# Kernel optimization log

Hardware: AMD Instinct MI355X
Metric: run time of the kernel (lower is better)

Reference implementation:

```python
import jax, jax.numpy as jnp
import numpy as np

INPUT_SIZE = 300
HIDDEN = 128
NUM_CLASSES = 2
B, T = 256, 512


def setup_inputs() -> dict:
    key = jax.random.key(0)
    ks = jax.random.split(key, 7)
    s_ih = 1.0 / np.sqrt(HIDDEN)
    x = jax.random.normal(ks[0], (B, T, INPUT_SIZE), dtype=jnp.float32)
    W_ih = jax.random.uniform(ks[1], (HIDDEN, INPUT_SIZE), minval=-s_ih, maxval=s_ih, dtype=jnp.float32)
    W_hh = jax.random.uniform(ks[2], (HIDDEN, HIDDEN), minval=-s_ih, maxval=s_ih, dtype=jnp.float32)
    b_ih = jax.random.uniform(ks[3], (HIDDEN,), minval=-s_ih, maxval=s_ih, dtype=jnp.float32)
    b_hh = jax.random.uniform(ks[4], (HIDDEN,), minval=-s_ih, maxval=s_ih, dtype=jnp.float32)
    fc_w = jax.random.uniform(ks[5], (NUM_CLASSES, HIDDEN), minval=-s_ih, maxval=s_ih, dtype=jnp.float32)
    fc_b = jax.random.uniform(ks[6], (NUM_CLASSES,), minval=-s_ih, maxval=s_ih, dtype=jnp.float32)
    return {"x": x, "W_ih": W_ih, "W_hh": W_hh, "b_ih": b_ih, "b_hh": b_hh, "fc_w": fc_w, "fc_b": fc_b}


def reference(x, W_ih, W_hh, b_ih, b_hh, fc_w, fc_b):
    # Precompute input projections for all timesteps: [B,T,H]
    xp = jnp.einsum('bti,hi->bth', x, W_ih) + b_ih + b_hh
    h0 = jnp.zeros((x.shape[0], HIDDEN), dtype=x.dtype)

    def step(h, xp_t):  # xp_t: [B,H]
        h_new = jnp.tanh(xp_t + h @ W_hh.T)
        return h_new, None

    h_last, _ = jax.lax.scan(step, h0, jnp.swapaxes(xp, 0, 1))  # scan over T
    # Final FC on last hidden state (out[:, -1, :] of the RNN outputs)
    return h_last @ fc_w.T + fc_b
```

## Files before the change

kernel.cpp:

```cpp
#include <hip/hip_runtime.h>
#include <cstdint>
#include <cstddef>

#define KIN 300
#define KPAD 320
#define HIDDEN 128
#define BSZ 256
#define TSZ 512

#define ASTR 332

typedef __attribute__((ext_vector_type(8))) short short8;
typedef __attribute__((ext_vector_type(4))) short s16x4;
typedef __attribute__((ext_vector_type(4))) float f32x4;

__device__ __forceinline__ short f2bf(float f) {
  uint32_t u = __builtin_bit_cast(uint32_t, f);
  u = (u + 0x7FFFu + ((u >> 16) & 1u)) >> 16;
  return (short)u;
}
__device__ __forceinline__ float bf2f(short s) {
  uint32_t u = ((uint32_t)(uint16_t)s) << 16;
  return __builtin_bit_cast(float, u);
}
__device__ __forceinline__ float bflo(uint32_t u) {
  return __builtin_bit_cast(float, u << 16);
}
__device__ __forceinline__ float bfhi(uint32_t u) {
  return __builtin_bit_cast(float, u & 0xFFFF0000u);
}
__device__ __forceinline__ uint32_t pack2bf(float a, float b) {
  uint32_t r;
  asm("v_cvt_pk_bf16_f32 %0, %1, %2" : "=v"(r) : "v"(a), "v"(b));
  return r;
}
__device__ __forceinline__ float tanhf_fast(float v) {
  const float e = __builtin_amdgcn_exp2f(v * 2.88539008177793f);
  return fmaf(-2.0f, __builtin_amdgcn_rcpf(e + 1.0f), 1.0f);
}
__device__ __forceinline__ void barrier_lds() {
  asm volatile("s_waitcnt lgkmcnt(0)\n\ts_barrier" ::: "memory");
}
__device__ __forceinline__ void barrier_all() {
  asm volatile("s_waitcnt vmcnt(0) lgkmcnt(0)\n\ts_barrier" ::: "memory");
}
__device__ __forceinline__ void dma16(const short* g, short* l) {
  __builtin_amdgcn_global_load_lds(
      (const __attribute__((address_space(1))) void*)g,
      (__attribute__((address_space(3))) void*)l, 16, 0, 0);
}
__device__ __forceinline__ short8 ld_bh(const short* lo) {
  const s16x4 a = *(const s16x4*)lo;
  const s16x4 b = *(const s16x4*)(lo + 64);
  return __builtin_shufflevector(a, b, 0, 1, 2, 3, 4, 5, 6, 7);
}

__global__ __launch_bounds__(256) void wcvt_bf16(const float* __restrict__ W,
                                                 short* __restrict__ W16) {
  const int i = blockIdx.x * 256 + threadIdx.x;
  if (i >= HIDDEN * KPAD) return;
  const int n = i / KPAD, k = i % KPAD;
  W16[i] = (k < KIN) ? f2bf(W[n * KIN + k]) : (short)0;
}

__global__ __launch_bounds__(256) void xp_gemm_mfma(
    const float* __restrict__ x, const short* __restrict__ W16,
    const float* __restrict__ b_ih, const float* __restrict__ b_hh,
    short* __restrict__ xp16) {
  __shared__ __align__(16) short As[64 * ASTR];
  const int tid = threadIdx.x;
  const int lane = tid & 63, w = tid >> 6;
  const int q = lane >> 4, c = lane & 15;
  const int bg = blockIdx.x & 15, tc = blockIdx.x >> 4;
  const int b0 = bg * 16, t0 = tc * 4;

#pragma unroll
  for (int i = 0; i < 19; ++i) {
    const int f = tid + 256 * i;
    if (f < 4800) {
      const int rr = f / 75;
      const int k4 = f - rr * 75;
      const int b_in = rr >> 2, t_loc = rr & 3;
      const float4 v = *(const float4*)(
          x + ((size_t)(b0 + b_in) * TSZ + t0 + t_loc) * KIN + k4 * 4);
      uint2 pv;
      pv.x = pack2bf(v.x, v.y);
      pv.y = pack2bf(v.z, v.w);
      *(uint2*)&As[rr * ASTR + k4 * 4] = pv;
    }
  }
  if (tid < 64) {
    const uint2 z = {0u, 0u};
#pragma unroll
    for (int j = 0; j < 5; ++j) *(uint2*)&As[tid * ASTR + 300 + j * 4] = z;
  }
  __syncthreads();

  f32x4 acc[2][4];
#pragma unroll
  for (int ht = 0; ht < 2; ++ht)
#pragma unroll
    for (int rt = 0; rt < 4; ++rt) acc[ht][rt] = (f32x4){0.f, 0.f, 0.f, 0.f};

  const short* wp0 = W16 + (size_t)((2 * w + 0) * 16 + c) * KPAD + q * 8;
  const short* wp1 = W16 + (size_t)((2 * w + 1) * 16 + c) * KPAD + q * 8;
  const short* bqp = &As[c * ASTR + q * 8];
  short8 af[2][2];
  short8 bq[2][4];
  af[0][0] = *(const short8*)(wp0);
  af[0][1] = *(const short8*)(wp1);
#pragma unroll
  for (int rt = 0; rt < 4; ++rt)
    bq[0][rt] = *(const short8*)(bqp + rt * 16 * ASTR);
#pragma unroll
  for (int kc = 0; kc < 10; ++kc) {
    const int cur = kc & 1;
    if (kc < 9) {
      af[cur ^ 1][0] = *(const short8*)(wp0 + (kc + 1) * 32);
      af[cur ^ 1][1] = *(const short8*)(wp1 + (kc + 1) * 32);
#pragma unroll
      for (int rt = 0; rt < 4; ++rt)
        bq[cur ^ 1][rt] = *(const short8*)(bqp + rt * 16 * ASTR + (kc + 1) * 32);
    }
#pragma unroll
    for (int ht = 0; ht < 2; ++ht)
#pragma unroll
      for (int rt = 0; rt < 4; ++rt)
        acc[ht][rt] = __builtin_amdgcn_mfma_f32_16x16x32_bf16(
            af[cur][ht], bq[cur][rt], acc[ht][rt], 0, 0, 0);
  }
  __syncthreads();

  float4 bsum[2];
#pragma unroll
  for (int ht = 0; ht < 2; ++ht) {
    const int h0 = (2 * w + ht) * 16 + q * 4;
    const float4 bi = *(const float4*)(b_ih + h0);
    const float4 bh = *(const float4*)(b_hh + h0);
    bsum[ht] = make_float4(bi.x + bh.x, bi.y + bh.y, bi.z + bh.z, bi.w + bh.w);
  }
#pragma unroll
  for (int ht = 0; ht < 2; ++ht) {
    const int g = (2 * w + ht) * 4 + q;
#pragma unroll
    for (int rt = 0; rt < 4; ++rt) {
      const int b_in = rt * 4 + (c >> 2);
      const int t_loc = c & 3;
      uint2 pv;
      pv.x = pack2bf(acc[ht][rt][0] + bsum[ht].x, acc[ht][rt][1] + bsum[ht].y);
      pv.y = pack2bf(acc[ht][rt][2] + bsum[ht].z, acc[ht][rt][3] + bsum[ht].w);
      *(uint2*)&As[t_loc * 2312 + g * 72 + b_in * 4] = pv;
    }
  }
  __syncthreads();
#pragma unroll
  for (int i = 0; i < 4; ++i) {
    const int4 vv =
        *(const int4*)&As[i * 2312 + (tid >> 3) * 72 + (tid & 7) * 8];
    *(int4*)(xp16 + ((size_t)(t0 + i) * 16 + bg) * 2048 + tid * 8) = vv;
  }
}

__global__ __launch_bounds__(512, 2) void rnn_scan_dma(
    const short* __restrict__ xp16, const float* __restrict__ Whh,
    const float* __restrict__ fc_w, const float* __restrict__ fc_b,
    float* __restrict__ out) {
  __shared__ __align__(16) short xs[2][8][2048];
  __shared__ __align__(16) short ht[2][16][132];
  const int tid = threadIdx.x;
  const int lane = tid & 63, w = tid >> 6;
  const int q = lane >> 4, c = lane & 15;
  const int bg = blockIdx.x;

  short8 aw[4];
#pragma unroll
  for (int kc = 0; kc < 4; ++kc) {
    const float* src = Whh + (size_t)(w * 16 + c) * HIDDEN + kc * 32 + q * 8;
    const float4 v0 = *(const float4*)(src);
    const float4 v1 = *(const float4*)(src + 4);
    short8 t;
    t[0] = f2bf(v0.x); t[1] = f2bf(v0.y); t[2] = f2bf(v0.z); t[3] = f2bf(v0.w);
    t[4] = f2bf(v1.x); t[5] = f2bf(v1.y); t[6] = f2bf(v1.z); t[7] = f2bf(v1.w);
    aw[kc] = t;
  }

  {
    uint32_t* z = (uint32_t*)&ht[0][0][0];
    for (int i = tid; i < 2112; i += 512) z[i] = 0;
  }

#define ISSUE_CHUNK(CH, BUF)                                                  \
  {                                                                           \
    const short* srcb =                                                       \
        xp16 + ((size_t)((CH)*8 + w) * 16 + bg) * 2048 + lane * 8;            \
    _Pragma("unroll") for (int j = 0; j < 4; ++j)                             \
        dma16(srcb + j * 512, &xs[BUF][w][j * 512]);                          \
  }

  ISSUE_CHUNK(0, 0)
  barrier_all();

  const int gx = (w * 4 + q) * 64 + c * 4;
  const int cb = (q & 1) * 64 + (2 * w + (q >> 1)) * 4;
  const short* bhp0 = &ht[0][c][4 * q];
  const short* bhp1 = &ht[1][c][4 * q];

  for (int cc = 0; cc < 64; ++cc) {
    const int buf = cc & 1;
    if (cc + 1 < 64) ISSUE_CHUNK(cc + 1, buf ^ 1)
    uint2 us[8];
#pragma unroll
    for (int s = 0; s < 8; ++s) us[s] = *(const uint2*)&xs[buf][s][gx];
#pragma unroll
    for (int s = 0; s < 8; ++s) {
      const int rb = s & 1;
      const short* bp = rb ? bhp1 : bhp0;
      const short8 bh0 = ld_bh(bp + 0);
      const short8 bh1 = ld_bh(bp + 16);
      const short8 bh2 = ld_bh(bp + 32);
      const short8 bh3 = ld_bh(bp + 48);
      f32x4 a0 = {bflo(us[s].x), bfhi(us[s].x), bflo(us[s].y), bfhi(us[s].y)};
      f32x4 a2 = {0.f, 0.f, 0.f, 0.f};
      a0 = __builtin_amdgcn_mfma_f32_16x16x32_bf16(aw[0], bh0, a0, 0, 0, 0);
      a2 = __builtin_amdgcn_mfma_f32_16x16x32_bf16(aw[2], bh2, a2, 0, 0, 0);
      a0 = __builtin_amdgcn_mfma_f32_16x16x32_bf16(aw[1], bh1, a0, 0, 0, 0);
      a2 = __builtin_amdgcn_mfma_f32_16x16x32_bf16(aw[3], bh3, a2, 0, 0, 0);
      const f32x4 s0 = a0 + a2;
      uint2 w0;
      w0.x = pack2bf(tanhf_fast(s0[0]), tanhf_fast(s0[1]));
      w0.y = pack2bf(tanhf_fast(s0[2]), tanhf_fast(s0[3]));
      *(uint2*)&ht[rb ^ 1][c][cb] = w0;
      barrier_lds();
    }
    barrier_all();
  }
#undef ISSUE_CHUNK

  if (tid < 32) {
    const int bi = tid >> 1, cls = tid & 1;
    float s = fc_b[cls];
    const float* fw = fc_w + cls * HIDDEN;
#pragma unroll 4
    for (int g8 = 0; g8 < 16; ++g8) {
#pragma unroll
      for (int j = 0; j < 4; ++j) {
        s = fmaf(bf2f(ht[0][bi][g8 * 4 + j]), fw[g8 * 8 + j], s);
        s = fmaf(bf2f(ht[0][bi][64 + g8 * 4 + j]), fw[g8 * 8 + 4 + j], s);
      }
    }
    out[(bg * 16 + bi) * 2 + cls] = s;
  }
}

extern "C" void kernel_launch(void* const* d_in, const int* in_sizes, int n_in,
                              void* d_out, int out_size, void* d_ws, size_t ws_size,
                              hipStream_t stream) {
  const float* x    = (const float*)d_in[0];
  const float* W_ih = (const float*)d_in[1];
  const float* W_hh = (const float*)d_in[2];
  const float* b_ih = (const float*)d_in[3];
  const float* b_hh = (const float*)d_in[4];
  const float* fc_w = (const float*)d_in[5];
  const float* fc_b = (const float*)d_in[6];
  short* xp16 = (short*)d_ws;
  short* W16  = (short*)((char*)d_ws + (33u << 20));
  float* out  = (float*)d_out;

  wcvt_bf16<<<(HIDDEN * KPAD + 255) / 256, 256, 0, stream>>>(W_ih, W16);
  xp_gemm_mfma<<<16 * (TSZ / 4), 256, 0, stream>>>(x, W16, b_ih, b_hh, xp16);
  rnn_scan_dma<<<16, 512, 0, stream>>>(xp16, W_hh, fc_w, fc_b, out);
}
```

Baseline: 445.9 us.

## Fuse input projection GEMM and RNN scan into one kernel with flag handoff

After: 533.6 us. 19.7% more time.

```diff
diff --git a/kernel.cpp b/kernel.cpp
--- a/kernel.cpp
+++ b/kernel.cpp
@@ -41,9 +41,6 @@
 __device__ __forceinline__ void barrier_lds() {
   asm volatile("s_waitcnt lgkmcnt(0)\n\ts_barrier" ::: "memory");
 }
-__device__ __forceinline__ void barrier_all() {
-  asm volatile("s_waitcnt vmcnt(0) lgkmcnt(0)\n\ts_barrier" ::: "memory");
-}
 __device__ __forceinline__ void dma16(const short* g, short* l) {
   __builtin_amdgcn_global_load_lds(
       (const __attribute__((address_space(1))) void*)g,
@@ -54,123 +51,136 @@
   const s16x4 b = *(const s16x4*)(lo + 64);
   return __builtin_shufflevector(a, b, 0, 1, 2, 3, 4, 5, 6, 7);
 }
-
-__global__ __launch_bounds__(256) void wcvt_bf16(const float* __restrict__ W,
-                                                 short* __restrict__ W16) {
-  const int i = blockIdx.x * 256 + threadIdx.x;
-  if (i >= HIDDEN * KPAD) return;
-  const int n = i / KPAD, k = i % KPAD;
-  W16[i] = (k < KIN) ? f2bf(W[n * KIN + k]) : (short)0;
-}
-
-__global__ __launch_bounds__(256) void xp_gemm_mfma(
-    const float* __restrict__ x, const short* __restrict__ W16,
-    const float* __restrict__ b_ih, const float* __restrict__ b_hh,
-    short* __restrict__ xp16) {
-  __shared__ __align__(16) short As[64 * ASTR];
+__device__ __forceinline__ short8 ldWfrag(const float* __restrict__ W, int row,
+                                          int k0) {
+  short8 t;
+  const float* p = W + (size_t)row * KIN + k0;
+  if (k0 + 8 <= KIN) {
+    const float4 v0 = *(const float4*)(p);
+    const float4 v1 = *(const float4*)(p + 4);
+    t[0] = f2bf(v0.x); t[1] = f2bf(v0.y); t[2] = f2bf(v0.z); t[3] = f2bf(v0.w);
+    t[4] = f2bf(v1.x); t[5] = f2bf(v1.y); t[6] = f2bf(v1.z); t[7] = f2bf(v1.w);
+  } else {
+#pragma unroll
+    for (int j = 0; j < 8; ++j) {
+      const int k = k0 + j;
+      t[j] = (k < KIN) ? f2bf(p[j]) : (short)0;
+    }
+  }
+  return t;
+}
+
+union SMemU {
+  short As[64 * ASTR];
+  struct {
+    short xs[3][8][2048];
+    short ht[2][16][132];
+  } c;
+};
+
+__global__ __launch_bounds__(512, 1) void rnn_fused(
+    const float* __restrict__ x, const float* __restrict__ Wih,
+    const float* __restrict__ Whh, const float* __restrict__ b_ih,
+    const float* __restrict__ b_hh, const float* __restrict__ fc_w,
+    const float* __restrict__ fc_b, short* __restrict__ xp16,
+    int* __restrict__ flags, float* __restrict__ out) {
+  __shared__ __align__(16) union SMemU sm;
   const int tid = threadIdx.x;
   const int lane = tid & 63, w = tid >> 6;
   const int q = lane >> 4, c = lane & 15;
-  const int bg = blockIdx.x & 15, tc = blockIdx.x >> 4;
-  const int b0 = bg * 16, t0 = tc * 4;
-
-#pragma unroll
-  for (int i = 0; i < 19; ++i) {
-    const int f = tid + 256 * i;
-    if (f < 4800) {
-      const int rr = f / 75;
-      const int k4 = f - rr * 75;
-      const int b_in = rr >> 2, t_loc = rr & 3;
-      const float4 v = *(const float4*)(
-          x + ((size_t)(b0 + b_in) * TSZ + t0 + t_loc) * KIN + k4 * 4);
-      uint2 pv;
-      pv.x = pack2bf(v.x, v.y);
-      pv.y = pack2bf(v.z, v.w);
-      *(uint2*)&As[rr * ASTR + k4 * 4] = pv;
-    }
-  }
-  if (tid < 64) {
-    const uint2 z = {0u, 0u};
-#pragma unroll
-    for (int j = 0; j < 5; ++j) *(uint2*)&As[tid * ASTR + 300 + j * 4] = z;
-  }
-  __syncthreads();
-
-  f32x4 acc[2][4];
-#pragma unroll
-  for (int ht = 0; ht < 2; ++ht)
-#pragma unroll
-    for (int rt = 0; rt < 4; ++rt) acc[ht][rt] = (f32x4){0.f, 0.f, 0.f, 0.f};
-
-  const short* wp0 = W16 + (size_t)((2 * w + 0) * 16 + c) * KPAD + q * 8;
-  const short* wp1 = W16 + (size_t)((2 * w + 1) * 16 + c) * KPAD + q * 8;
-  const short* bqp = &As[c * ASTR + q * 8];
-  short8 af[2][2];
-  short8 bq[2][4];
-  af[0][0] = *(const short8*)(wp0);
-  af[0][1] = *(const short8*)(wp1);
-#pragma unroll
-  for (int rt = 0; rt < 4; ++rt)
-    bq[0][rt] = *(const short8*)(bqp + rt * 16 * ASTR);
-#pragma unroll
-  for (int kc = 0; kc < 10; ++kc) {
-    const int cur = kc & 1;
-    if (kc < 9) {
-      af[cur ^ 1][0] = *(const short8*)(wp0 + (kc + 1) * 32);
-      af[cur ^ 1][1] = *(const short8*)(wp1 + (kc + 1) * 32);
+
+  if (blockIdx.x >= 16) {
+    const int pid = blockIdx.x - 16;
+    const int bg = pid & 15, tc = pid >> 4;
+    const int b0 = bg * 16, t0 = tc * 4;
+    short* As = sm.As;
+
+#pragma unroll
+    for (int i = 0; i < 10; ++i) {
+      const int f = tid + 512 * i;
+      if (f < 4800) {
+        const int rr = f / 75;
+        const int k4 = f - rr * 75;
+        const int b_in = rr >> 2, t_loc = rr & 3;
+        const float4 v = *(const float4*)(
+            x + ((size_t)(b0 + b_in) * TSZ + t0 + t_loc) * KIN + k4 * 4);
+        uint2 pv;
+        pv.x = pack2bf(v.x, v.y);
+        pv.y = pack2bf(v.z, v.w);
+        *(uint2*)&As[rr * ASTR + k4 * 4] = pv;
+      }
+    }
+    if (tid < 64) {
+      const uint2 z = {0u, 0u};
+#pragma unroll
+      for (int j = 0; j < 5; ++j) *(uint2*)&As[tid * ASTR + 300 + j * 4] = z;
+    }
+    __syncthreads();
+
+    f32x4 acc[4];
+#pragma unroll
+    for (int rt = 0; rt < 4; ++rt) acc[rt] = (f32x4){0.f, 0.f, 0.f, 0.f};
+    const int row = w * 16 + c;
+    const short* bqp = &As[c * ASTR + q * 8];
+    short8 af[2];
+    short8 bq[2][4];
+    af[0] = ldWfrag(Wih, row, q * 8);
+#pragma unroll
+    for (int rt = 0; rt < 4; ++rt)
+      bq[0][rt] = *(const short8*)(bqp + rt * 16 * ASTR);
+#pragma unroll
+    for (int kc = 0; kc < 10; ++kc) {
+      const int cur = kc & 1;
+      if (kc < 9) {
+        af[cur ^ 1] = ldWfrag(Wih, row, (kc + 1) * 32 + q * 8);
+#pragma unroll
+        for (int rt = 0; rt < 4; ++rt)
+          bq[cur ^ 1][rt] =
+              *(const short8*)(bqp + rt * 16 * ASTR + (kc + 1) * 32);
+      }
 #pragma unroll
       for (int rt = 0; rt < 4; ++rt)
-        bq[cur ^ 1][rt] = *(const short8*)(bqp + rt * 16 * ASTR + (kc + 1) * 32);
-    }
-#pragma unroll
-    for (int ht = 0; ht < 2; ++ht)
-#pragma unroll
-      for (int rt = 0; rt < 4; ++rt)
-        acc[ht][rt] = __builtin_amdgcn_mfma_f32_16x16x32_bf16(
-            af[cur][ht], bq[cur][rt], acc[ht][rt], 0, 0, 0);
-  }
-  __syncthreads();
-
-  float4 bsum[2];
-#pragma unroll
-  for (int ht = 0; ht < 2; ++ht) {
-    const int h0 = (2 * w + ht) * 16 + q * 4;
+        acc[rt] = __builtin_amdgcn_mfma_f32_16x16x32_bf16(af[cur], bq[cur][rt],
+                                                          acc[rt], 0, 0, 0);
+    }
+    __syncthreads();
+
+    const int h0 = w * 16 + q * 4;
     const float4 bi = *(const float4*)(b_ih + h0);
     const float4 bh = *(const float4*)(b_hh + h0);
-    bsum[ht] = make_float4(bi.x + bh.x, bi.y + bh.y, bi.z + bh.z, bi.w + bh.w);
-  }
-#pragma unroll
-  for (int ht = 0; ht < 2; ++ht) {
-    const int g = (2 * w + ht) * 4 + q;
+    const float4 bsum =
+        make_float4(bi.x + bh.x, bi.y + bh.y, bi.z + bh.z, bi.w + bh.w);
+    const int g = w * 4 + q;
 #pragma unroll
     for (int rt = 0; rt < 4; ++rt) {
       const int b_in = rt * 4 + (c >> 2);
       const int t_loc = c & 3;
       uint2 pv;
-      pv.x = pack2bf(acc[ht][rt][0] + bsum[ht].x, acc[ht][rt][1] + bsum[ht].y);
-      pv.y = pack2bf(acc[ht][rt][2] + bsum[ht].z, acc[ht][rt][3] + bsum[ht].w);
+      pv.x = pack2bf(acc[rt][0] + bsum.x, acc[rt][1] + bsum.y);
+      pv.y = pack2bf(acc[rt][2] + bsum.z, acc[rt][3] + bsum.w);
       *(uint2*)&As[t_loc * 2312 + g * 72 + b_in * 4] = pv;
     }
-  }
-  __syncthreads();
-#pragma unroll
-  for (int i = 0; i < 4; ++i) {
-    const int4 vv =
-        *(const int4*)&As[i * 2312 + (tid >> 3) * 72 + (tid & 7) * 8];
-    *(int4*)(xp16 + ((size_t)(t0 + i) * 16 + bg) * 2048 + tid * 8) = vv;
-  }
-}
-
-__global__ __launch_bounds__(512, 2) void rnn_scan_dma(
-    const short* __restrict__ xp16, const float* __restrict__ Whh,
-    const float* __restrict__ fc_w, const float* __restrict__ fc_b,
-    float* __restrict__ out) {
-  __shared__ __align__(16) short xs[2][8][2048];
-  __shared__ __align__(16) short ht[2][16][132];
-  const int tid = threadIdx.x;
-  const int lane = tid & 63, w = tid >> 6;
-  const int q = lane >> 4, c = lane & 15;
+    __syncthreads();
+#pragma unroll
+    for (int i = 0; i < 2; ++i) {
+      const int t_loc = i * 2 + (tid >> 8);
+      const int inner = tid & 255;
+      const int4 vv =
+          *(const int4*)&As[t_loc * 2312 + (inner >> 3) * 72 + (inner & 7) * 8];
+      *(int4*)(xp16 + ((size_t)(t0 + t_loc) * 16 + bg) * 2048 + inner * 8) = vv;
+    }
+    __syncthreads();
+    if (tid == 0) {
+      __builtin_amdgcn_fence(__ATOMIC_RELEASE, "agent");
+      __hip_atomic_fetch_add(&flags[bg * 64 + (tc >> 1)], 1, __ATOMIC_RELAXED,
+                             __HIP_MEMORY_SCOPE_AGENT);
+    }
+    return;
+  }
+
   const int bg = blockIdx.x;
+  short(*xs)[8][2048] = sm.c.xs;
+  short(*ht)[16][132] = sm.c.ht;
 
   short8 aw[4];
 #pragma unroll
@@ -189,28 +199,48 @@
     for (int i = tid; i < 2112; i += 512) z[i] = 0;
   }
 
-#define ISSUE_CHUNK(CH, BUF)                                                  \
+  int* flg = flags + bg * 64;
+  int ni = 0, ib = 0, fv = 0;
+#define GATE()                                                                \
   {                                                                           \
+    while (fv < 2) {                                                          \
+      if (lane == 0)                                                          \
+        fv = __hip_atomic_load(flg + ni, __ATOMIC_RELAXED,                    \
+                               __HIP_MEMORY_SCOPE_AGENT);                     \
+      fv = __builtin_amdgcn_readfirstlane(fv);                                \
+      if (fv < 2) __builtin_amdgcn_s_sleep(8);                                \
+    }                                                                         \
+    __builtin_amdgcn_fence(__ATOMIC_ACQUIRE, "agent");                        \
     const short* srcb =                                                       \
-        xp16 + ((size_t)((CH)*8 + w) * 16 + bg) * 2048 + lane * 8;            \
+        xp16 + ((size_t)(ni * 8 + w) * 16 + bg) * 2048 + lane * 8;            \
     _Pragma("unroll") for (int j = 0; j < 4; ++j)                             \
-        dma16(srcb + j * 512, &xs[BUF][w][j * 512]);                          \
-  }
-
-  ISSUE_CHUNK(0, 0)
-  barrier_all();
+        dma16(srcb + j * 512, &xs[ib][w][j * 512]);                           \
+    ni++;                                                                     \
+    ib = (ib == 2) ? 0 : ib + 1;                                              \
+    fv = (ni < 64) ? 0 : 2;                                                   \
+    if (ni < 64) {                                                            \
+      if (lane == 0)                                                          \
+        fv = __hip_atomic_load(flg + ni, __ATOMIC_RELAXED,                    \
+                               __HIP_MEMORY_SCOPE_AGENT);                     \
+      fv = __builtin_amdgcn_readfirstlane(fv);                                \
+    }                                                                         \
+  }
+
+  GATE();
+  GATE();
+  asm volatile("s_waitcnt vmcnt(4) lgkmcnt(0)\n\ts_barrier" ::: "memory");
 
   const int gx = (w * 4 + q) * 64 + c * 4;
   const int cb = (q & 1) * 64 + (2 * w + (q >> 1)) * 4;
   const short* bhp0 = &ht[0][c][4 * q];
   const short* bhp1 = &ht[1][c][4 * q];
+  int rb3 = 0;
 
   for (int cc = 0; cc < 64; ++cc) {
-    const int buf = cc & 1;
-    if (cc + 1 < 64) ISSUE_CHUNK(cc + 1, buf ^ 1)
+    if (cc + 2 < 64) GATE()
     uint2 us[8];
 #pragma unroll
-    for (int s = 0; s < 8; ++s) us[s] = *(const uint2*)&xs[buf][s][gx];
+    for (int s = 0; s < 8; ++s) us[s] = *(const uint2*)&xs[rb3][s][gx];
 #pragma unroll
     for (int s = 0; s < 8; ++s) {
       const int rb = s & 1;
@@ -232,9 +262,13 @@
       *(uint2*)&ht[rb ^ 1][c][cb] = w0;
       barrier_lds();
     }
-    barrier_all();
-  }
-#undef ISSUE_CHUNK
+    if (cc + 2 < 64)
+      asm volatile("s_waitcnt vmcnt(4) lgkmcnt(0)\n\ts_barrier" ::: "memory");
+    else
+      asm volatile("s_waitcnt vmcnt(0) lgkmcnt(0)\n\ts_barrier" ::: "memory");
+    rb3 = (rb3 == 2) ? 0 : rb3 + 1;
+  }
+#undef GATE
 
   if (tid < 32) {
     const int bi = tid >> 1, cls = tid & 1;
@@ -263,10 +297,10 @@
   const float* fc_w = (const float*)d_in[5];
   const float* fc_b = (const float*)d_in[6];
   short* xp16 = (short*)d_ws;
-  short* W16  = (short*)((char*)d_ws + (33u << 20));
+  int* flags  = (int*)((char*)d_ws + (33u << 20));
   float* out  = (float*)d_out;
 
-  wcvt_bf16<<<(HIDDEN * KPAD + 255) / 256, 256, 0, stream>>>(W_ih, W16);
-  xp_gemm_mfma<<<16 * (TSZ / 4), 256, 0, stream>>>(x, W16, b_ih, b_hh, xp16);
-  rnn_scan_dma<<<16, 512, 0, stream>>>(xp16, W_hh, fc_w, fc_b, out);
-}
+  hipMemsetAsync(flags, 0, 16 * 64 * sizeof(int), stream);
+  rnn_fused<<<16 + 16 * (TSZ / 4), 512, 0, stream>>>(
+      x, W_ih, W_hh, b_ih, b_hh, fc_w, fc_b, xp16, flags, out);
+}
```
